# Performance work log

Hardware: AMD Instinct MI355X
Metric: run time of the kernel (lower is better)

## Reference

```python
import jax, jax.numpy as jnp
import numpy as np

B, C, H, W = 16, 512, 64, 64
C1 = C // (C // 256)  # 256: conv output channels, per scale = in_dim // 256


def setup_inputs() -> dict:
    key = jax.random.key(0)
    k1, k2, k3, k4 = jax.random.split(key, 4)
    x = jax.random.normal(k1, (B, C, H, W), dtype=jnp.float32)
    # 1x1 conv params (kaiming-ish scale for C fan-in)
    conv_w = jax.random.normal(k2, (C1, C, 1, 1), dtype=jnp.float32) * (1.0 / np.sqrt(C))
    conv_b = jax.random.normal(k3, (C1,), dtype=jnp.float32) * 0.01
    # gamma is nn.Parameter(zeros(1)) in torch; use a random value so the
    # attention branch actually contributes to the output under test.
    gamma = jax.random.normal(k4, (1,), dtype=jnp.float32)
    return {"x": x, "conv_w": conv_w, "conv_b": conv_b, "gamma": gamma}


def reference(x, conv_w, conv_b, gamma):
    b, c, h, w = x.shape
    hw = h * w
    # 1x1 conv == channel-mixing matmul
    proj_query = jnp.einsum('bchw,oc->bohw', x, conv_w[:, :, 0, 0]) + conv_b[None, :, None, None]
    xres = proj_query                     # residual (B, C1, H, W)
    c1 = proj_query.shape[1]
    q = proj_query.reshape(b, c1, hw)     # (B, C1, HW)
    k = x.reshape(b, c, hw)               # (B, C,  HW)
    # einsum 'ijk,iklm->ijlm' over (B,HW,8,C/8) then view back == q @ k^T
    energy = jnp.einsum('bqn,bcn->bqc', q, k) / jnp.asarray(np.sqrt(hw), x.dtype)
    attention = jax.nn.softmax(energy, axis=-1)   # (B, C1, C), softmax over C
    out = jnp.einsum('bqc,bcn->bqn', attention, k).reshape(b, c1, h, w)
    return gamma * out + xres
```

## Files before the change

### kernel.cpp

```cpp
#include <hip/hip_runtime.h>
#include <stdint.h>

#define B_  16
#define C_  512
#define C1_ 256
#define HW_ 4096

using bf16x8 = __attribute__((ext_vector_type(8))) short;
using f32x4  = __attribute__((ext_vector_type(4))) float;

__device__ __forceinline__ short f2bf(float f) {
  union { float f; unsigned int u; } v; v.f = f;
  unsigned int r = v.u + 0x7fffu + ((v.u >> 16) & 1u);
  return (short)(r >> 16);
}
__device__ __forceinline__ float bf2f(short s) {
  union { unsigned int u; float f; } v;
  v.u = ((unsigned int)(unsigned short)s) << 16;
  return v.f;
}

__device__ __forceinline__ void gload_lds16(const void* g, void* l) {
  __builtin_amdgcn_global_load_lds(
      (const __attribute__((address_space(1))) void*)g,
      (__attribute__((address_space(3))) void*)l, 16, 0, 0);
}

__global__ __launch_bounds__(256) void k_copy(const float* __restrict__ x,
                                              short* __restrict__ Xbf) {
  const size_t stride = (size_t)gridDim.x * 256;
  size_t tid = (size_t)blockIdx.x * 256 + threadIdx.x;
#pragma unroll
  for (int p = 0; p < 8; ++p) {
    const size_t idx = (tid + p * stride) * 8;
    const float4 v0 = *(const float4*)(x + idx);
    const float4 v1 = *(const float4*)(x + idx + 4);
    bf16x8 o;
    o[0] = f2bf(v0.x); o[1] = f2bf(v0.y); o[2] = f2bf(v0.z); o[3] = f2bf(v0.w);
    o[4] = f2bf(v1.x); o[5] = f2bf(v1.y); o[6] = f2bf(v1.z); o[7] = f2bf(v1.w);
    *(bf16x8*)(Xbf + idx) = o;
  }
}

__global__ __launch_bounds__(256) void k_transpose(const short* __restrict__ Xbf,
                                                   short* __restrict__ XbfT) {
  __shared__ short T[64][72];
  const int n0 = blockIdx.x * 64, c0 = blockIdx.y * 64, b = blockIdx.z;
  const int t = threadIdx.x;
  const int nc = (t & 7) * 8;
  const int cr = t >> 3;
#pragma unroll
  for (int it = 0; it < 2; ++it) {
    const int c = cr + it * 32;
    const bf16x8 v = *(const bf16x8*)(Xbf + ((size_t)(b * C_ + c0 + c)) * HW_ + n0 + nc);
    *(bf16x8*)&T[c][nc] = v;
  }
  __syncthreads();
  const int cc = (t & 7) * 8;
  const int np = t >> 3;
  bf16x8 oa, ob;
#pragma unroll
  for (int e = 0; e < 8; ++e) {
    const short2 pr = *(const short2*)&T[cc + e][2 * np];
    oa[e] = pr.x; ob[e] = pr.y;
  }
  short* o0 = XbfT + ((size_t)b * HW_ + n0 + 2 * np) * C_ + c0 + cc;
  *(bf16x8*)(o0)      = oa;
  *(bf16x8*)(o0 + C_) = ob;
}

__global__ __launch_bounds__(256) void k_wconv(const float* __restrict__ W,
                                               short* __restrict__ Wbf) {
  const int q = blockIdx.x, t = threadIdx.x;
  const float2 v = ((const float2*)(W + (size_t)q * C_))[t];
  short2 o; o.x = f2bf(v.x); o.y = f2bf(v.y);
  ((short2*)(Wbf + (size_t)q * C_))[t] = o;
}

template<int KITER, int LDK>
__device__ __forceinline__ void nt_loop(const short* __restrict__ Ab,
                                        const short* __restrict__ Bb,
                                        short* As, short* Bs, int t,
                                        f32x4 (&acc)[4][4]) {
  const int lane = t & 63, w = t >> 6;
  const int wr = w >> 1, wc = w & 1;
  const int fr = lane & 15, fk = (lane >> 4) * 8;
  const int row_st = t >> 2, k_st = (t & 3) * 8;

#define STAGE_(buf, kk)                                                         \
  {                                                                             \
    const int k0_ = (kk) * 32 + k_st;                                           \
    gload_lds16(Ab + (size_t)row_st * LDK + k0_, As + (buf) * 4096 + t * 8);    \
    gload_lds16(Ab + (size_t)(row_st + 64) * LDK + k0_,                         \
                As + (buf) * 4096 + 2048 + t * 8);                              \
    gload_lds16(Bb + (size_t)row_st * LDK + k0_, Bs + (buf) * 4096 + t * 8);    \
    gload_lds16(Bb + (size_t)(row_st + 64) * LDK + k0_,                         \
                Bs + (buf) * 4096 + 2048 + t * 8);                              \
  }

  STAGE_(0, 0);
  asm volatile("s_waitcnt vmcnt(0)" ::: "memory");
  __builtin_amdgcn_s_barrier();
  int cur = 0;
  for (int kk = 0; kk < KITER; ++kk) {
    if (kk + 1 < KITER) STAGE_(cur ^ 1, kk + 1);
    const short* Ac = As + cur * 4096;
    const short* Bc = Bs + cur * 4096;
    bf16x8 a[4], bv[4];
#pragma unroll
    for (int m = 0; m < 4; ++m)
      a[m] = *(const bf16x8*)&Ac[(wr * 64 + m * 16 + fr) * 32 + fk];
#pragma unroll
    for (int n = 0; n < 4; ++n)
      bv[n] = *(const bf16x8*)&Bc[(wc * 64 + n * 16 + fr) * 32 + fk];
#pragma unroll
    for (int m = 0; m < 4; ++m)
#pragma unroll
      for (int n = 0; n < 4; ++n)
        acc[m][n] = __builtin_amdgcn_mfma_f32_16x16x32_bf16(a[m], bv[n], acc[m][n], 0, 0, 0);
    asm volatile("s_waitcnt vmcnt(0) lgkmcnt(0)" ::: "memory");
    __builtin_amdgcn_s_barrier();
    cur ^= 1;
  }
#undef STAGE_
}

__global__ __launch_bounds__(256, 2) void k_q(const short* __restrict__ Wbf,
                                              const short* __restrict__ XbfT,
                                              const float* __restrict__ convb,
                                              short* __restrict__ Qbf) {
  __shared__ short As[2 * 4096];
  __shared__ short Bs[2 * 4096];
  const int t = threadIdx.x;
  const int mt = blockIdx.x & 1, nt = blockIdx.x >> 1, b = blockIdx.y;
  const short* Ab = Wbf + (size_t)(mt * 128) * C_;
  const short* Bb = XbfT + ((size_t)b * HW_ + nt * 128) * C_;
  f32x4 acc[4][4] = {};
  nt_loop<16, C_>(Ab, Bb, As, Bs, t, acc);
  const int lane = t & 63, w = t >> 6;
  const int wr = w >> 1, wc = w & 1;
  const int q_base = mt * 128 + wr * 64;
  const int n_base = nt * 128 + wc * 64;
#pragma unroll
  for (int m = 0; m < 4; ++m)
#pragma unroll
    for (int n = 0; n < 4; ++n) {
      const int q = q_base + m * 16 + (lane >> 4) * 4;
      const int nn = n_base + n * 16 + (lane & 15);
#pragma unroll
      for (int r = 0; r < 4; ++r)
        Qbf[((size_t)b * C1_ + q + r) * HW_ + nn] = f2bf(acc[m][n][r] + convb[q + r]);
    }
}

template<int KITER>
__global__ __launch_bounds__(256, 2) void k_e(const short* __restrict__ Qbf,
                                              const short* __restrict__ Xbf,
                                              short* __restrict__ Ep) {
  __shared__ short As[2 * 4096];
  __shared__ short Bs[2 * 4096];
  const int t = threadIdx.x;
  const int b = blockIdx.x;
  const int qt = blockIdx.y & 1, ct = blockIdx.y >> 1;
  const int ks = blockIdx.z;
  const short* Ab = Qbf + ((size_t)b * C1_ + qt * 128) * HW_ + (size_t)ks * (KITER * 32);
  const short* Bb = Xbf + ((size_t)b * C_ + ct * 128) * HW_ + (size_t)ks * (KITER * 32);
  f32x4 acc[4][4] = {};
  nt_loop<KITER, HW_>(Ab, Bb, As, Bs, t, acc);
  const int lane = t & 63, w = t >> 6;
  const int wr = w >> 1, wc = w & 1;
  const int q_base = qt * 128 + wr * 64;
  const int c_base = ct * 128 + wc * 64;
#pragma unroll
  for (int m = 0; m < 4; ++m)
#pragma unroll
    for (int n = 0; n < 4; ++n) {
      const int q = q_base + m * 16 + (lane >> 4) * 4;
      const int c = c_base + n * 16 + (lane & 15);
#pragma unroll
      for (int r = 0; r < 4; ++r)
        Ep[(((size_t)ks * B_ + b) * C1_ + q + r) * C_ + c] = f2bf(acc[m][n][r]);
    }
}

template<int NKS>
__global__ __launch_bounds__(128) void k_softmax(const short* __restrict__ Ep,
                                                 const float* __restrict__ W,
                                                 const float* __restrict__ gamma,
                                                 short* __restrict__ Mb) {
  const int bq = blockIdx.x;
  const int b = bq >> 8, q = bq & 255;
  const int t = threadIdx.x;
  const float g = gamma[0];
  float e[4] = {0.f, 0.f, 0.f, 0.f};
#pragma unroll
  for (int ks = 0; ks < NKS; ++ks) {
    const short4 v = *(const short4*)&Ep[(((size_t)ks * B_ + b) * C1_ + q) * C_ + t * 4];
    e[0] += bf2f(v.x); e[1] += bf2f(v.y); e[2] += bf2f(v.z); e[3] += bf2f(v.w);
  }
#pragma unroll
  for (int d = 0; d < 4; ++d) e[d] *= 0.015625f;
  float mx = fmaxf(fmaxf(e[0], e[1]), fmaxf(e[2], e[3]));
#pragma unroll
  for (int off = 1; off < 64; off <<= 1) mx = fmaxf(mx, __shfl_xor(mx, off));
  __shared__ float red[2];
  if ((t & 63) == 0) red[t >> 6] = mx;
  __syncthreads();
  mx = fmaxf(red[0], red[1]);
  const float e0 = __expf(e[0] - mx), e1 = __expf(e[1] - mx);
  const float e2 = __expf(e[2] - mx), e3 = __expf(e[3] - mx);
  float sum = (e0 + e1) + (e2 + e3);
#pragma unroll
  for (int off = 1; off < 64; off <<= 1) sum += __shfl_xor(sum, off);
  __shared__ float red2[2];
  if ((t & 63) == 0) red2[t >> 6] = sum;
  __syncthreads();
  const float inv = 1.0f / (red2[0] + red2[1]);
  const float4 wv = ((const float4*)(W + (size_t)q * C_))[t];
  short4 o;
  o.x = f2bf(g * e0 * inv + wv.x);
  o.y = f2bf(g * e1 * inv + wv.y);
  o.z = f2bf(g * e2 * inv + wv.z);
  o.w = f2bf(g * e3 * inv + wv.w);
  ((short4*)(Mb + (size_t)bq * C_))[t] = o;
}

__global__ __launch_bounds__(256, 2) void k_out(const short* __restrict__ Mb,
                                                const short* __restrict__ XbfT,
                                                const float* __restrict__ convb,
                                                float* __restrict__ out) {
  __shared__ short As[2 * 4096];
  __shared__ short Bs[2 * 4096];
  const int t = threadIdx.x;
  const int mt = blockIdx.x & 1, nt = blockIdx.x >> 1, b = blockIdx.y;
  const short* Ab = Mb + ((size_t)b * C1_ + mt * 128) * C_;
  const short* Bb = XbfT + ((size_t)b * HW_ + nt * 128) * C_;
  f32x4 acc[4][4] = {};
  nt_loop<16, C_>(Ab, Bb, As, Bs, t, acc);
  const int lane = t & 63, w = t >> 6;
  const int wr = w >> 1, wc = w & 1;
  const int o_base = mt * 128 + wr * 64;
  const int n_base = nt * 128 + wc * 64;
#pragma unroll
  for (int m = 0; m < 4; ++m)
#pragma unroll
    for (int n = 0; n < 4; ++n) {
      const int oo = o_base + m * 16 + (lane >> 4) * 4;
      const int nn = n_base + n * 16 + (lane & 15);
#pragma unroll
      for (int r = 0; r < 4; ++r)
        out[((size_t)b * C1_ + oo + r) * HW_ + nn] = acc[m][n][r] + convb[oo + r];
    }
}

extern "C" void kernel_launch(void* const* d_in, const int* in_sizes, int n_in,
                              void* d_out, int out_size, void* d_ws, size_t ws_size,
                              hipStream_t stream) {
  const float* x      = (const float*)d_in[0];
  const float* conv_w = (const float*)d_in[1];
  const float* conv_b = (const float*)d_in[2];
  const float* gamma  = (const float*)d_in[3];
  float* out = (float*)d_out;

  char* ws = (char*)d_ws;
  short* Xbf  = (short*)(ws);
  short* XbfT = (short*)(ws + 67108864);
  short* Qbf  = (short*)(ws + 134217728);
  short* Mb   = (short*)(ws + 134217728);
  short* Ep   = (short*)(ws + 167772160);
  const bool big = ws_size >= 201588736ull;
  short* Wbf  = (short*)(ws + (big ? 201326592u : 184549376u));

  k_copy<<<2048, 256, 0, stream>>>(x, Xbf);
  k_transpose<<<dim3(64, 8, 16), 256, 0, stream>>>(Xbf, XbfT);
  k_wconv<<<256, 256, 0, stream>>>(conv_w, Wbf);
  k_q<<<dim3(64, 16), 256, 0, stream>>>(Wbf, XbfT, conv_b, Qbf);
  if (big) {
    k_e<16><<<dim3(16, 8, 8), 256, 0, stream>>>(Qbf, Xbf, Ep);
    k_softmax<8><<<4096, 128, 0, stream>>>(Ep, conv_w, gamma, Mb);
  } else {
    k_e<32><<<dim3(16, 8, 4), 256, 0, stream>>>(Qbf, Xbf, Ep);
    k_softmax<4><<<4096, 128, 0, stream>>>(Ep, conv_w, gamma, Mb);
  }
  k_out<<<dim3(64, 16), 256, 0, stream>>>(Mb, XbfT, conv_b, out);
}
```

Baseline: 166.2 us.

## Restructure transpose to full-row tiles and raise GEMM occupancy bound

The transpose kernel now stages a 32-position by 512-channel tile in shared memory, so each output row of XbfT is written as a full contiguous 1 KB row instead of two 16-byte chunks per row. Shared-memory writes become scalar scattered stores, which adds bank conflicts in exchange for fully coalesced global writes. Separately, the three GEMM kernels raise their launch-bounds minimum blocks per CU from 2 to 3, which may let more waves overlap memory latency but can force register spilling.

```diff
diff --git a/kernel.cpp b/kernel.cpp
--- a/kernel.cpp
+++ b/kernel.cpp
@@ -44,29 +44,26 @@
 
 __global__ __launch_bounds__(256) void k_transpose(const short* __restrict__ Xbf,
                                                    short* __restrict__ XbfT) {
-  __shared__ short T[64][72];
-  const int n0 = blockIdx.x * 64, c0 = blockIdx.y * 64, b = blockIdx.z;
-  const int t = threadIdx.x;
-  const int nc = (t & 7) * 8;
-  const int cr = t >> 3;
-#pragma unroll
-  for (int it = 0; it < 2; ++it) {
-    const int c = cr + it * 32;
-    const bf16x8 v = *(const bf16x8*)(Xbf + ((size_t)(b * C_ + c0 + c)) * HW_ + n0 + nc);
-    *(bf16x8*)&T[c][nc] = v;
+  __shared__ short T[32][520];
+  const int n0 = blockIdx.x * 32, b = blockIdx.y;
+  const int t = threadIdx.x;
+#pragma unroll
+  for (int i = 0; i < 8; ++i) {
+    const int u = i * 256 + t;
+    const int c = u >> 2;
+    const int nc = u & 3;
+    const bf16x8 v = *(const bf16x8*)(Xbf + ((size_t)(b * C_ + c)) * HW_ + n0 + nc * 8);
+#pragma unroll
+    for (int j = 0; j < 8; ++j) T[nc * 8 + j][c] = v[j];
   }
   __syncthreads();
-  const int cc = (t & 7) * 8;
-  const int np = t >> 3;
-  bf16x8 oa, ob;
-#pragma unroll
-  for (int e = 0; e < 8; ++e) {
-    const short2 pr = *(const short2*)&T[cc + e][2 * np];
-    oa[e] = pr.x; ob[e] = pr.y;
-  }
-  short* o0 = XbfT + ((size_t)b * HW_ + n0 + 2 * np) * C_ + c0 + cc;
-  *(bf16x8*)(o0)      = oa;
-  *(bf16x8*)(o0 + C_) = ob;
+  const int lane = t & 63, w = t >> 6;
+#pragma unroll
+  for (int r = 0; r < 8; ++r) {
+    const int n = w * 8 + r;
+    const bf16x8 v = *(const bf16x8*)&T[n][lane * 8];
+    *(bf16x8*)(XbfT + ((size_t)b * HW_ + n0 + n) * C_ + lane * 8) = v;
+  }
 }
 
 __global__ __launch_bounds__(256) void k_wconv(const float* __restrict__ W,
@@ -125,7 +122,7 @@
 #undef STAGE_
 }
 
-__global__ __launch_bounds__(256, 2) void k_q(const short* __restrict__ Wbf,
+__global__ __launch_bounds__(256, 3) void k_q(const short* __restrict__ Wbf,
                                               const short* __restrict__ XbfT,
                                               const float* __restrict__ convb,
                                               short* __restrict__ Qbf) {
@@ -154,7 +151,7 @@
 }
 
 template<int KITER>
-__global__ __launch_bounds__(256, 2) void k_e(const short* __restrict__ Qbf,
+__global__ __launch_bounds__(256, 3) void k_e(const short* __restrict__ Qbf,
                                               const short* __restrict__ Xbf,
                                               short* __restrict__ Ep) {
   __shared__ short As[2 * 4096];
@@ -225,7 +222,7 @@
   ((short4*)(Mb + (size_t)bq * C_))[t] = o;
 }
 
-__global__ __launch_bounds__(256, 2) void k_out(const short* __restrict__ Mb,
+__global__ __launch_bounds__(256, 3) void k_out(const short* __restrict__ Mb,
                                                 const short* __restrict__ XbfT,
                                                 const float* __restrict__ convb,
                                                 float* __restrict__ out) {
@@ -272,7 +269,7 @@
   short* Wbf  = (short*)(ws + (big ? 201326592u : 184549376u));
 
   k_copy<<<2048, 256, 0, stream>>>(x, Xbf);
-  k_transpose<<<dim3(64, 8, 16), 256, 0, stream>>>(Xbf, XbfT);
+  k_transpose<<<dim3(128, 16), 256, 0, stream>>>(Xbf, XbfT);
   k_wconv<<<256, 256, 0, stream>>>(conv_w, Wbf);
   k_q<<<dim3(64, 16), 256, 0, stream>>>(Wbf, XbfT, conv_b, Qbf);
   if (big) {
```

Result: slower. 184.2 us (+10.8%).
